# Kernel optimization log

Measured on AMD Instinct MI355X. Metric: run time of the kernel, lower is better.

## Reference

```python
import jax, jax.numpy as jnp
import numpy as np

CHANNELS = 256
NUM_HEADS = 4
NUM_GROUPS = 8
EPS = 1e-5


def setup_inputs() -> dict:
    key = jax.random.key(0)
    ks = jax.random.split(key, 7)
    c = CHANNELS
    x = jax.random.normal(ks[0], (2, c, 16, 16, 16), dtype=jnp.float32)
    # GroupNorm affine params (torch init: weight=1, bias=0)
    norm_w = jnp.ones((c,), dtype=jnp.float32)
    norm_b = jnp.zeros((c,), dtype=jnp.float32)
    # 1x1x1 Conv3d weights stored as [out_ch, in_ch]
    fan = 1.0 / np.sqrt(c)
    qkv_w = jax.random.uniform(ks[1], (3 * c, c), minval=-fan, maxval=fan, dtype=jnp.float32)
    qkv_b = jax.random.uniform(ks[2], (3 * c,), minval=-fan, maxval=fan, dtype=jnp.float32)
    proj_w = jax.random.uniform(ks[3], (c, c), minval=-fan, maxval=fan, dtype=jnp.float32)
    proj_b = jax.random.uniform(ks[4], (c,), minval=-fan, maxval=fan, dtype=jnp.float32)
    return {"x": x, "norm_w": norm_w, "norm_b": norm_b,
            "qkv_w": qkv_w, "qkv_b": qkv_b, "proj_w": proj_w, "proj_b": proj_b}


def _group_norm(x, w, b):
    B, C, D, H, W = x.shape
    g = NUM_GROUPS
    xg = x.reshape(B, g, C // g, D, H, W)
    mean = xg.mean(axis=(2, 3, 4, 5), keepdims=True)
    var = xg.var(axis=(2, 3, 4, 5), keepdims=True)
    xg = (xg - mean) * jax.lax.rsqrt(var + EPS)
    x = xg.reshape(B, C, D, H, W)
    return x * w[None, :, None, None, None] + b[None, :, None, None, None]


def _conv1x1(x, w, b):
    # x: [B, Cin, D, H, W], w: [Cout, Cin]
    y = jnp.einsum('bcdhw,oc->bodhw', x, w)
    return y + b[None, :, None, None, None]


def reference(x, norm_w, norm_b, qkv_w, qkv_b, proj_w, proj_b):
    B, C, D, H, W = x.shape
    N = D * H * W
    hd = C // NUM_HEADS
    x_norm = _group_norm(x, norm_w, norm_b)
    qkv = _conv1x1(x_norm, qkv_w, qkv_b)  # [B, 3C, D, H, W]
    q, k, v = jnp.split(qkv, 3, axis=1)
    q = q.reshape(B, NUM_HEADS, hd, N)
    k = k.reshape(B, NUM_HEADS, hd, N)
    v = v.reshape(B, NUM_HEADS, hd, N)
    scale = hd ** -0.5
    # attn[b,h,n,m] = softmax_m(q[:, :, :, n] . k[:, :, :, m] * scale)
    scores = jnp.einsum('bhcn,bhcm->bhnm', q, k) * scale
    attn = jax.nn.softmax(scores, axis=-1)
    out = jnp.einsum('bhcm,bhnm->bhcn', v, attn)
    out = out.reshape(B, C, D, H, W)
    return _conv1x1(out, proj_w, proj_b) + x
```

## Files before the change

### kernel.cpp

```cpp
#include <hip/hip_runtime.h>
#include <hip/hip_bf16.h>

#define NSP 4096
#define CH 256
#define NB 2
#define NG 8
#define CPG 32
#define NHD 4
#define HDIM 64

typedef unsigned short u16;
typedef unsigned int u32;
typedef __attribute__((ext_vector_type(8))) short bf16x8;
typedef __attribute__((ext_vector_type(2))) float f32x2;
typedef __attribute__((ext_vector_type(4))) float f32x4;
typedef __attribute__((ext_vector_type(16))) float f32x16;
typedef __attribute__((ext_vector_type(2))) unsigned int u32x2;

#define MFMA __builtin_amdgcn_mfma_f32_16x16x32_bf16
#define MFMA32 __builtin_amdgcn_mfma_f32_32x32x16_bf16
#define QSCALE 0.18033688f

__device__ __forceinline__ u16 f2bf(float f) {
    u32 i = __float_as_uint(f);
    u32 r = (i + 0x7FFFu + ((i >> 16) & 1u)) >> 16;
    return (u16)r;
}

__device__ __forceinline__ u32 cvtpk(float a, float b) {
    u32 d;
    asm("v_cvt_pk_bf16_f32 %0, %1, %2" : "=v"(d) : "v"(a), "v"(b));
    return d;
}

__device__ __forceinline__ void dma16(const u16* g, u16* l) {
    __builtin_amdgcn_global_load_lds(
        (const __attribute__((address_space(1))) void*)g,
        (__attribute__((address_space(3))) void*)l, 16, 0, 0);
}

__device__ __forceinline__ void plswap(u32& a, u32& b) {
#if __has_builtin(__builtin_amdgcn_permlane32_swap)
    u32x2 r = __builtin_amdgcn_permlane32_swap(a, b, false, false);
    a = r.x; b = r.y;
#else
    u32 sa = (u32)__shfl_xor((int)a, 32);
    u32 sb = (u32)__shfl_xor((int)b, 32);
    bool hi = (threadIdx.x & 32) != 0;
    u32 na = hi ? sb : a;
    u32 nb = hi ? b : sa;
    a = na; b = nb;
#endif
}

__global__ __launch_bounds__(256) void prep(const float* __restrict__ qw,
                                            const float* __restrict__ pw,
                                            u16* __restrict__ wqb,
                                            u16* __restrict__ wpb,
                                            const float* __restrict__ x,
                                            float* __restrict__ partial) {
    if (blockIdx.x < 256) {
        int i = (blockIdx.x * 256 + threadIdx.x) * 4;
        const float* src; u16* dstbase; int j;
        if (i < 3 * CH * CH) { src = qw + i; dstbase = wqb; j = i; }
        else { j = i - 3 * CH * CH; src = pw + j; dstbase = wpb; }
        int m = j >> 8, c = j & 255;
        int dc = ((((c >> 3) ^ (m & 7)) << 3)) | (c & 7);
        float4 v = *(const float4*)src;
        ushort4 o;
        o.x = f2bf(v.x); o.y = f2bf(v.y); o.z = f2bf(v.z); o.w = f2bf(v.w);
        *(ushort4*)(dstbase + (m << 8) + dc) = o;
        return;
    }
    const int id = blockIdx.x - 256;
    const int bg = id >> 4, chunk = id & 15;
    const float* p = x + (size_t)bg * (CPG * NSP) + chunk * 8192;
    float s = 0.f, ss = 0.f;
    for (int i = threadIdx.x; i < 2048; i += 256) {
        float4 u = ((const float4*)p)[i];
        s += u.x + u.y + u.z + u.w;
        ss += u.x * u.x + u.y * u.y + u.z * u.z + u.w * u.w;
    }
    for (int off = 32; off > 0; off >>= 1) {
        s += __shfl_down(s, off);
        ss += __shfl_down(ss, off);
    }
    __shared__ float red[4][2];
    const int wv = threadIdx.x >> 6;
    if ((threadIdx.x & 63) == 0) { red[wv][0] = s; red[wv][1] = ss; }
    __syncthreads();
    if (threadIdx.x == 0) {
        float ts = red[0][0] + red[1][0] + red[2][0] + red[3][0];
        float tq = red[0][1] + red[1][1] + red[2][1] + red[3][1];
        partial[(bg * 16 + chunk) * 2]     = ts;
        partial[(bg * 16 + chunk) * 2 + 1] = tq;
    }
}

__global__ __launch_bounds__(256) void gn_apply_t(const float* __restrict__ x,
                                                  const float* __restrict__ partial,
                                                  const float* __restrict__ w,
                                                  const float* __restrict__ b,
                                                  u16* __restrict__ xnT) {
    __shared__ u16 T[64][72];
    const int n0 = blockIdx.x * 64, c0 = blockIdx.y * 64, bb = blockIdx.z;
    const int t = threadIdx.x;
    const int rc = t & 63;
    const int g  = t >> 6;
    const int c  = c0 + rc;
    const int bg = bb * NG + c / CPG;
    float s = 0.f, q = 0.f;
#pragma unroll
    for (int j = 0; j < 16; ++j) {
        s += partial[(bg * 16 + j) * 2];
        q += partial[(bg * 16 + j) * 2 + 1];
    }
    const float cnt = (float)(CPG * NSP);
    float mean = s / cnt;
    float var  = q / cnt - mean * mean;
    float rstd = rsqrtf(var + 1e-5f);
    float wf = w[c] * rstd, bv = b[c] - mean * wf;
    const float* px = x + ((size_t)bb * CH + c) * NSP + n0 + g * 16;
#pragma unroll
    for (int i = 0; i < 4; ++i) {
        float4 v = *(const float4*)(px + i * 4);
        T[g * 16 + i * 4 + 0][rc] = f2bf(v.x * wf + bv);
        T[g * 16 + i * 4 + 1][rc] = f2bf(v.y * wf + bv);
        T[g * 16 + i * 4 + 2][rc] = f2bf(v.z * wf + bv);
        T[g * 16 + i * 4 + 3][rc] = f2bf(v.w * wf + bv);
    }
    __syncthreads();
    int n = t >> 2, ch = (t & 3) * 16;
    uint4 o0 = *(const uint4*)&T[n][ch];
    uint4 o1 = *(const uint4*)&T[n][ch + 8];
    const int sw = n & 7;
    const int chunk0 = (c0 + ch) >> 3;
    u16* rowp = xnT + ((size_t)bb * NSP + n0 + n) * CH;
    *(uint4*)(rowp + ((chunk0 ^ sw) << 3))       = o0;
    *(uint4*)(rowp + (((chunk0 + 1) ^ sw) << 3)) = o1;
}

__global__ __launch_bounds__(256, 2) void gemm_qkv(const u16* __restrict__ Aw,
                                                   const float* __restrict__ bias,
                                                   const u16* __restrict__ xnT,
                                                   u16* __restrict__ qT,
                                                   u16* __restrict__ kT,
                                                   u16* __restrict__ v) {
    __shared__ u16 As[64][256];
    __shared__ u16 Bs[64][256];
    const int flat = blockIdx.x + 64 * (blockIdx.y + 12 * blockIdx.z);
    const int xcd = flat & 7, loc = flat >> 3;
    const int mI  = loc % 12;
    const int n16 = xcd * 16 + loc / 12;
    const int n0 = (n16 & 63) * 64, m0 = mI * 64, bb = n16 >> 6;
    const int wave = threadIdx.x >> 6, lane = threadIdx.x & 63;
    const int lq = lane & 15, quad = lane >> 4;
#pragma unroll
    for (int j = 0; j < 8; ++j) {
        int r2 = (wave * 8 + j) * 2;
        dma16(Aw + (size_t)(m0 + r2) * CH + lane * 8, &As[r2][0]);
        dma16(xnT + ((size_t)bb * NSP + n0 + r2) * CH + lane * 8, &Bs[r2][0]);
    }
    __syncthreads();
    const int wm = (wave >> 1) * 32, wn = (wave & 1) * 32;
    const int sw = lq & 7;
    f32x4 acc[2][2] = {};
#pragma unroll
    for (int kk = 0; kk < 8; ++kk) {
        bf16x8 a[2], b[2];
#pragma unroll
        for (int mt = 0; mt < 2; ++mt)
            a[mt] = *(const bf16x8*)&As[wm + mt * 16 + lq][(((kk * 4 + quad) ^ sw)) << 3];
#pragma unroll
        for (int nt = 0; nt < 2; ++nt)
            b[nt] = *(const bf16x8*)&Bs[wn + nt * 16 + lq][(((kk * 4 + quad) ^ sw)) << 3];
#pragma unroll
        for (int mt = 0; mt < 2; ++mt)
#pragma unroll
            for (int nt = 0; nt < 2; ++nt)
                acc[mt][nt] = MFMA(a[mt], b[nt], acc[mt][nt], 0, 0, 0);
    }
    const int sect = m0 >> 8;
    const int h = (m0 & 255) >> 6;
    const float osc = (sect == 0) ? QSCALE : 1.f;
#pragma unroll
    for (int im = 0; im < 2; ++im) {
        int ml = wm + im * 16 + quad * 4;
        float4 bs = *(const float4*)(bias + m0 + ml);
#pragma unroll
        for (int in = 0; in < 2; ++in) {
            int n = n0 + wn + in * 16 + lq;
            f32x4 a = acc[im][in];
            float v0 = (a[0] + bs.x) * osc, v1 = (a[1] + bs.y) * osc;
            float v2 = (a[2] + bs.z) * osc, v3 = (a[3] + bs.w) * osc;
            if (sect < 2) {
                int lc = ml >> 3, sub = ml & 7;
                int colp = ((lc ^ (n & 7)) << 3) | sub;
                u16* base = (sect ? kT : qT) +
                            (((size_t)bb * NHD + h) * NSP + n) * HDIM + colp;
                ushort4 o;
                o.x = f2bf(v0); o.y = f2bf(v1); o.z = f2bf(v2); o.w = f2bf(v3);
                *(ushort4*)base = o;
            } else {
                float vv[4] = {v0, v1, v2, v3};
#pragma unroll
                for (int r = 0; r < 4; ++r) {
                    int ch = (m0 - 512) + ml + r;
                    int pos = (n & ~63) + ((((n >> 3) & 7) ^ (ch & 7)) << 3) + (n & 7);
                    v[((size_t)bb * CH + ch) * NSP + pos] = f2bf(vv[r]);
                }
            }
        }
    }
}

__global__ __launch_bounds__(512, 2) void attn16(const u16* __restrict__ qT,
                                                 const u16* __restrict__ kT,
                                                 const u16* __restrict__ vN,
                                                 u16* __restrict__ aoT) {
    __shared__ __align__(16) char smem[131072];
    u16 (*Ks)[2][64][64] = reinterpret_cast<u16(*)[2][64][64]>(smem);
    u16 (*Vs)[2][64][64] = reinterpret_cast<u16(*)[2][64][64]>(smem + 65536);

    const int id  = blockIdx.x + 32 * (blockIdx.y + 4 * blockIdx.z);
    const int xcd = id & 7, loc = id >> 3;
    const int h = xcd & 3, bb = xcd >> 2;

    const int t = threadIdx.x;
    const int wave = t >> 6, lane = t & 63;
    const int l31 = lane & 31, hi = lane >> 5, ln7 = lane & 7;
    const int qg = wave >> 2;
    const int csl = wave & 3;
    const int q_lo = loc * 128 + qg * 64;

    bf16x8 qf0[4], qf1[4];
    {
        const u16* qrow0 = qT + (((size_t)bb * NHD + h) * NSP + q_lo + l31) * HDIM;
        const u16* qrow1 = qrow0 + 32 * HDIM;
#pragma unroll
        for (int d = 0; d < 4; ++d) {
            qf0[d] = *(const bf16x8*)(qrow0 + (((d * 2 + hi) ^ ln7) << 3));
            qf1[d] = *(const bf16x8*)(qrow1 + (((d * 2 + hi) ^ ln7) << 3));
        }
    }

    const u16* khead = kT + ((size_t)bb * NHD + h) * NSP * (size_t)HDIM;
    const u16* vhead = vN + ((size_t)bb * CH + h * HDIM) * NSP;

    const int sV  = wave >> 2;
    const int ssl = wave & 3;
    int koff[4];
#pragma unroll
    for (int d = 0; d < 4; ++d) koff[d] = (((d * 2 + hi) ^ ln7) << 3);

#pragma unroll
    for (int j = 0; j < 8; ++j) {
        if (sV == 0)
            dma16(khead + (size_t)(ssl * 1024 + j * 8) * HDIM + lane * 8,
                  &Ks[ssl][0][j * 8][0]);
        else
            dma16(vhead + (size_t)(j * 8 + (lane >> 3)) * NSP + ssl * 1024 + (lane & 7) * 8,
                  &Vs[ssl][0][j * 8][0]);
    }

    float l0 = 0.f, l1 = 0.f;
    f32x16 O00 = {}, O01 = {}, O10 = {}, O11 = {};

    auto softmax_pack = [&](const f32x16& s, float& lacc, u32* pfa, u32* pfb) {
        f32x2 a2 = {0.f, 0.f};
        u32 pk0, pk1, pk2, pk3, pk4, pk5, pk6, pk7;
        {
            float p0 = __builtin_amdgcn_exp2f(s[0]),  p1 = __builtin_amdgcn_exp2f(s[1]);
            float p2 = __builtin_amdgcn_exp2f(s[2]),  p3 = __builtin_amdgcn_exp2f(s[3]);
            a2 += (f32x2){p0, p1}; a2 += (f32x2){p2, p3};
            pk0 = cvtpk(p0, p1); pk1 = cvtpk(p2, p3);
        }
        {
            float p0 = __builtin_amdgcn_exp2f(s[4]),  p1 = __builtin_amdgcn_exp2f(s[5]);
            float p2 = __builtin_amdgcn_exp2f(s[6]),  p3 = __builtin_amdgcn_exp2f(s[7]);
            a2 += (f32x2){p0, p1}; a2 += (f32x2){p2, p3};
            pk2 = cvtpk(p0, p1); pk3 = cvtpk(p2, p3);
        }
        {
            float p0 = __builtin_amdgcn_exp2f(s[8]),  p1 = __builtin_amdgcn_exp2f(s[9]);
            float p2 = __builtin_amdgcn_exp2f(s[10]), p3 = __builtin_amdgcn_exp2f(s[11]);
            a2 += (f32x2){p0, p1}; a2 += (f32x2){p2, p3};
            pk4 = cvtpk(p0, p1); pk5 = cvtpk(p2, p3);
        }
        {
            float p0 = __builtin_amdgcn_exp2f(s[12]), p1 = __builtin_amdgcn_exp2f(s[13]);
            float p2 = __builtin_amdgcn_exp2f(s[14]), p3 = __builtin_amdgcn_exp2f(s[15]);
            a2 += (f32x2){p0, p1}; a2 += (f32x2){p2, p3};
            pk6 = cvtpk(p0, p1); pk7 = cvtpk(p2, p3);
        }
        lacc += a2.x + a2.y;
        plswap(pk0, pk2); plswap(pk1, pk3);
        plswap(pk4, pk6); plswap(pk5, pk7);
        pfa[0] = pk0; pfa[1] = pk1; pfa[2] = pk2; pfa[3] = pk3;
        pfb[0] = pk4; pfb[1] = pk5; pfb[2] = pk6; pfb[3] = pk7;
    };

    for (int kt = 0; kt < 16; ++kt) {
        const int cur = kt & 1;
        __syncthreads();
        if (kt < 15) {
            const int K1 = (kt + 1) * 64;
#pragma unroll
            for (int j = 0; j < 8; ++j) {
                if (sV == 0)
                    dma16(khead + (size_t)(ssl * 1024 + K1 + j * 8) * HDIM + lane * 8,
                          &Ks[ssl][cur ^ 1][j * 8][0]);
                else
                    dma16(vhead + (size_t)(j * 8 + (lane >> 3)) * NSP + ssl * 1024 + K1 + (lane & 7) * 8,
                          &Vs[ssl][cur ^ 1][j * 8][0]);
            }
        }
        f32x16 st00 = {}, st01 = {}, st10 = {}, st11 = {};
        {
            bf16x8 kf0 = *(const bf16x8*)&Ks[csl][cur][l31][koff[0]];
            bf16x8 kf1 = *(const bf16x8*)&Ks[csl][cur][l31][koff[1]];
            bf16x8 kf2 = *(const bf16x8*)&Ks[csl][cur][l31][koff[2]];
            bf16x8 kf3 = *(const bf16x8*)&Ks[csl][cur][l31][koff[3]];
            st00 = MFMA32(kf0, qf0[0], st00, 0, 0, 0);
            st00 = MFMA32(kf1, qf0[1], st00, 0, 0, 0);
            st00 = MFMA32(kf2, qf0[2], st00, 0, 0, 0);
            st00 = MFMA32(kf3, qf0[3], st00, 0, 0, 0);
            st01 = MFMA32(kf0, qf1[0], st01, 0, 0, 0);
            st01 = MFMA32(kf1, qf1[1], st01, 0, 0, 0);
            st01 = MFMA32(kf2, qf1[2], st01, 0, 0, 0);
            st01 = MFMA32(kf3, qf1[3], st01, 0, 0, 0);
        }
        {
            bf16x8 kf0 = *(const bf16x8*)&Ks[csl][cur][32 + l31][koff[0]];
            bf16x8 kf1 = *(const bf16x8*)&Ks[csl][cur][32 + l31][koff[1]];
            bf16x8 kf2 = *(const bf16x8*)&Ks[csl][cur][32 + l31][koff[2]];
            bf16x8 kf3 = *(const bf16x8*)&Ks[csl][cur][32 + l31][koff[3]];
            st10 = MFMA32(kf0, qf0[0], st10, 0, 0, 0);
            st10 = MFMA32(kf1, qf0[1], st10, 0, 0, 0);
            st10 = MFMA32(kf2, qf0[2], st10, 0, 0, 0);
            st10 = MFMA32(kf3, qf0[3], st10, 0, 0, 0);
            st11 = MFMA32(kf0, qf1[0], st11, 0, 0, 0);
            st11 = MFMA32(kf1, qf1[1], st11, 0, 0, 0);
            st11 = MFMA32(kf2, qf1[2], st11, 0, 0, 0);
            st11 = MFMA32(kf3, qf1[3], st11, 0, 0, 0);
        }
#pragma unroll
        for (int ktile = 0; ktile < 2; ++ktile) {
            bf16x8 vf00 = *(const bf16x8*)&Vs[csl][cur][l31][(((ktile * 4 + hi) ^ ln7) << 3)];
            bf16x8 vf01 = *(const bf16x8*)&Vs[csl][cur][l31][(((ktile * 4 + 2 + hi) ^ ln7) << 3)];
            bf16x8 vf10 = *(const bf16x8*)&Vs[csl][cur][32 + l31][(((ktile * 4 + hi) ^ ln7) << 3)];
            bf16x8 vf11 = *(const bf16x8*)&Vs[csl][cur][32 + l31][(((ktile * 4 + 2 + hi) ^ ln7) << 3)];
            u32 pA0[4], pB0[4], pA1[4], pB1[4];
            softmax_pack(ktile ? st10 : st00, l0, pA0, pB0);
            softmax_pack(ktile ? st11 : st01, l1, pA1, pB1);
            bf16x8 a0 = *(const bf16x8*)pA0, b0 = *(const bf16x8*)pB0;
            bf16x8 a1 = *(const bf16x8*)pA1, b1 = *(const bf16x8*)pB1;
            O00 = MFMA32(vf00, a0, O00, 0, 0, 0);
            O00 = MFMA32(vf01, b0, O00, 0, 0, 0);
            O10 = MFMA32(vf00, a1, O10, 0, 0, 0);
            O10 = MFMA32(vf01, b1, O10, 0, 0, 0);
            O01 = MFMA32(vf10, a0, O01, 0, 0, 0);
            O01 = MFMA32(vf11, b0, O01, 0, 0, 0);
            O11 = MFMA32(vf10, a1, O11, 0, 0, 0);
            O11 = MFMA32(vf11, b1, O11, 0, 0, 0);
        }
    }
    l0 += __shfl_xor(l0, 32);
    l1 += __shfl_xor(l1, 32);
    __syncthreads();
    float* ob  = (float*)smem;
    float* MlA = (float*)(smem + 65536);
    if (lane < 32) {
        MlA[(wave * 2 + 0) * 32 + l31] = l0;
        MlA[(wave * 2 + 1) * 32 + l31] = l1;
    }
    auto stash = [&](float* sp, int f, const f32x16& o) {
#pragma unroll
        for (int cc = 0; cc < 4; ++cc) {
            f32x4 tmp = {o[4 * cc + 0], o[4 * cc + 1], o[4 * cc + 2], o[4 * cc + 3]};
            *(f32x4*)(sp + ((f * 4 + cc) * 64 + lane) * 4) = tmp;
        }
    };
    auto absorb = [&](const float* sp, int f, f32x16& o) {
#pragma unroll
        for (int cc = 0; cc < 4; ++cc) {
            f32x4 tmp = *(const f32x4*)(sp + ((f * 4 + cc) * 64 + lane) * 4);
            o[4 * cc + 0] += tmp[0]; o[4 * cc + 1] += tmp[1];
            o[4 * cc + 2] += tmp[2]; o[4 * cc + 3] += tmp[3];
        }
    };
    if (csl >= 2) {
        float* sp = ob + (qg * 2 + (csl - 2)) * 4096;
        stash(sp, 0, O00); stash(sp, 1, O01); stash(sp, 2, O10); stash(sp, 3, O11);
    }
    __syncthreads();
    if (csl < 2) {
        float* sp = ob + (qg * 2 + csl) * 4096;
        absorb(sp, 0, O00); absorb(sp, 1, O01); absorb(sp, 2, O10); absorb(sp, 3, O11);
    }
    __syncthreads();
    if (csl == 1) {
        float* sp = ob + qg * 4096;
        stash(sp, 0, O00); stash(sp, 1, O01); stash(sp, 2, O10); stash(sp, 3, O11);
    }
    __syncthreads();
    if (csl == 0) {
        float* sp = ob + qg * 4096;
        absorb(sp, 0, O00); absorb(sp, 1, O01); absorb(sp, 2, O10); absorb(sp, 3, O11);
        float gl0 = l0 + MlA[((qg * 4 + 1) * 2 + 0) * 32 + l31]
                       + MlA[((qg * 4 + 2) * 2 + 0) * 32 + l31]
                       + MlA[((qg * 4 + 3) * 2 + 0) * 32 + l31];
        float gl1 = l1 + MlA[((qg * 4 + 1) * 2 + 1) * 32 + l31]
                       + MlA[((qg * 4 + 2) * 2 + 1) * 32 + l31]
                       + MlA[((qg * 4 + 3) * 2 + 1) * 32 + l31];
        float linv0 = 1.f / gl0, linv1 = 1.f / gl1;
        auto emit = [&](const f32x16& oc0, const f32x16& oc1, float linv, int qtrow) {
            u16* rowp = aoT + ((size_t)bb * NSP + q_lo + qtrow * 32 + l31) * CH;
#pragma unroll
            for (int ct = 0; ct < 2; ++ct) {
                const f32x16& oc = ct ? oc1 : oc0;
#pragma unroll
                for (int g = 0; g < 4; ++g) {
                    ushort4 o;
                    o.x = f2bf(oc[4 * g + 0] * linv);
                    o.y = f2bf(oc[4 * g + 1] * linv);
                    o.z = f2bf(oc[4 * g + 2] * linv);
                    o.w = f2bf(oc[4 * g + 3] * linv);
                    int chunk = h * 8 + ct * 4 + g;
                    *(ushort4*)(rowp + ((chunk ^ ln7) << 3) + (hi << 2)) = o;
                }
            }
        };
        emit(O00, O01, linv0, 0);
        emit(O10, O11, linv1, 1);
    }
}

__global__ __launch_bounds__(256, 2) void gemm_proj(const u16* __restrict__ Aw,
                                                    const float* __restrict__ bias,
                                                    const u16* __restrict__ aoT,
                                                    const float* __restrict__ xres,
                                                    float* __restrict__ out) {
    __shared__ u16 As[64][256];
    __shared__ u16 Bs[64][256];
    const int flat = blockIdx.x + 64 * (blockIdx.y + 4 * blockIdx.z);
    const int xcd = flat & 7, loc = flat >> 3;
    const int mI  = loc & 3;
    const int n16 = xcd * 16 + (loc >> 2);
    const int n0 = (n16 & 63) * 64, m0 = mI * 64, bb = n16 >> 6;
    const int wave = threadIdx.x >> 6, lane = threadIdx.x & 63;
    const int lq = lane & 15, quad = lane >> 4;
#pragma unroll
    for (int j = 0; j < 8; ++j) {
        int r2 = (wave * 8 + j) * 2;
        dma16(Aw + (size_t)(m0 + r2) * CH + lane * 8, &As[r2][0]);
        dma16(aoT + ((size_t)bb * NSP + n0 + r2) * CH + lane * 8, &Bs[r2][0]);
    }
    __syncthreads();
    const int wm = (wave >> 1) * 32, wn = (wave & 1) * 32;
    const int sw = lq & 7;
    f32x4 acc[2][2] = {};
#pragma unroll
    for (int kk = 0; kk < 8; ++kk) {
        bf16x8 a[2], b[2];
#pragma unroll
        for (int mt = 0; mt < 2; ++mt)
            a[mt] = *(const bf16x8*)&As[wm + mt * 16 + lq][(((kk * 4 + quad) ^ sw)) << 3];
#pragma unroll
        for (int nt = 0; nt < 2; ++nt)
            b[nt] = *(const bf16x8*)&Bs[wn + nt * 16 + lq][(((kk * 4 + quad) ^ sw)) << 3];
#pragma unroll
        for (int mt = 0; mt < 2; ++mt)
#pragma unroll
            for (int nt = 0; nt < 2; ++nt)
                acc[mt][nt] = MFMA(a[mt], b[nt], acc[mt][nt], 0, 0, 0);
    }
#pragma unroll
    for (int im = 0; im < 2; ++im) {
        int ml = wm + im * 16 + quad * 4;
        float4 bs = *(const float4*)(bias + m0 + ml);
        float bsv[4] = {bs.x, bs.y, bs.z, bs.w};
#pragma unroll
        for (int in = 0; in < 2; ++in) {
            int n = n0 + wn + in * 16 + lq;
            f32x4 a = acc[im][in];
#pragma unroll
            for (int r = 0; r < 4; ++r) {
                size_t idx = ((size_t)bb * CH + m0 + ml + r) * NSP + n;
                out[idx] = a[r] + bsv[r] + xres[idx];
            }
        }
    }
}

extern "C" void kernel_launch(void* const* d_in, const int* in_sizes, int n_in,
                              void* d_out, int out_size, void* d_ws, size_t ws_size,
                              hipStream_t stream) {
    const float* x      = (const float*)d_in[0];
    const float* norm_w = (const float*)d_in[1];
    const float* norm_b = (const float*)d_in[2];
    const float* qkv_w  = (const float*)d_in[3];
    const float* qkv_b  = (const float*)d_in[4];
    const float* proj_w = (const float*)d_in[5];
    const float* proj_b = (const float*)d_in[6];
    float* out = (float*)d_out;

    char* w = (char*)d_ws;
    float* partial = (float*)w;
    u16* wqb = (u16*)(w + 4096);
    u16* wpb = (u16*)(w + 4096 + 393216);
    u16* xnT = (u16*)(w + 528384);
    u16* qT  = (u16*)(w + 528384 + 4194304);
    u16* kT  = (u16*)(w + 528384 + 2 * 4194304);
    u16* v   = (u16*)(w + 528384 + 3 * 4194304);
    u16* aoT = xnT;

    prep<<<dim3(512), 256, 0, stream>>>(qkv_w, proj_w, wqb, wpb, x, partial);
    gn_apply_t<<<dim3(NSP / 64, CH / 64, NB), 256, 0, stream>>>(
        x, partial, norm_w, norm_b, xnT);
    gemm_qkv<<<dim3(NSP / 64, (3 * CH) / 64, NB), 256, 0, stream>>>(
        wqb, qkv_b, xnT, qT, kT, v);
    attn16<<<dim3(NSP / 128, NHD, NB), 512, 0, stream>>>(qT, kT, v, aoT);
    gemm_proj<<<dim3(NSP / 64, CH / 64, NB), 256, 0, stream>>>(
        wpb, proj_b, aoT, x, out);
}
```

Before: 135.7 us.

## Split each attention wave's key tile across two waves in 1024-thread blocks

The attention kernel now launches 1024 threads per block instead of 512. Each pair of waves splits the 64-key tile into two 32-key halves, and the DMA load work is split between them. This halves per-wave score and softmax work and lowers register pressure, which is meant to improve latency hiding through more waves in flight. In exchange the cross-wave output reduction grows to three stash/absorb rounds with more barriers, and occupancy is bounded at one block per CU.

```diff
diff --git a/kernel.cpp b/kernel.cpp
--- a/kernel.cpp
+++ b/kernel.cpp
@@ -214,10 +214,10 @@
     }
 }
 
-__global__ __launch_bounds__(512, 2) void attn16(const u16* __restrict__ qT,
-                                                 const u16* __restrict__ kT,
-                                                 const u16* __restrict__ vN,
-                                                 u16* __restrict__ aoT) {
+__global__ __launch_bounds__(1024, 1) void attn17(const u16* __restrict__ qT,
+                                                  const u16* __restrict__ kT,
+                                                  const u16* __restrict__ vN,
+                                                  u16* __restrict__ aoT) {
     __shared__ __align__(16) char smem[131072];
     u16 (*Ks)[2][64][64] = reinterpret_cast<u16(*)[2][64][64]>(smem);
     u16 (*Vs)[2][64][64] = reinterpret_cast<u16(*)[2][64][64]>(smem + 65536);
@@ -229,8 +229,10 @@
     const int t = threadIdx.x;
     const int wave = t >> 6, lane = t & 63;
     const int l31 = lane & 31, hi = lane >> 5, ln7 = lane & 7;
-    const int qg = wave >> 2;
-    const int csl = wave & 3;
+    const int qg  = wave >> 3;
+    const int csl = (wave >> 1) & 3;
+    const int kth = wave & 1;
+    const int mi  = (csl << 1) | kth;
     const int q_lo = loc * 128 + qg * 64;
 
     bf16x8 qf0[4], qf1[4];
@@ -247,20 +249,22 @@
     const u16* khead = kT + ((size_t)bb * NHD + h) * NSP * (size_t)HDIM;
     const u16* vhead = vN + ((size_t)bb * CH + h * HDIM) * NSP;
 
-    const int sV  = wave >> 2;
-    const int ssl = wave & 3;
+    const int sV    = wave >> 3;
+    const int ssl   = (wave >> 1) & 3;
+    const int rbase = (wave & 1) * 32;
     int koff[4];
 #pragma unroll
     for (int d = 0; d < 4; ++d) koff[d] = (((d * 2 + hi) ^ ln7) << 3);
 
 #pragma unroll
-    for (int j = 0; j < 8; ++j) {
+    for (int j = 0; j < 4; ++j) {
+        int r8 = rbase + j * 8;
         if (sV == 0)
-            dma16(khead + (size_t)(ssl * 1024 + j * 8) * HDIM + lane * 8,
-                  &Ks[ssl][0][j * 8][0]);
+            dma16(khead + (size_t)(ssl * 1024 + r8) * HDIM + lane * 8,
+                  &Ks[ssl][0][r8][0]);
         else
-            dma16(vhead + (size_t)(j * 8 + (lane >> 3)) * NSP + ssl * 1024 + (lane & 7) * 8,
-                  &Vs[ssl][0][j * 8][0]);
+            dma16(vhead + (size_t)(r8 + (lane >> 3)) * NSP + ssl * 1024 + (lane & 7) * 8,
+                  &Vs[ssl][0][r8][0]);
     }
 
     float l0 = 0.f, l1 = 0.f;
@@ -306,74 +310,67 @@
         if (kt < 15) {
             const int K1 = (kt + 1) * 64;
 #pragma unroll
-            for (int j = 0; j < 8; ++j) {
+            for (int j = 0; j < 4; ++j) {
+                int r8 = rbase + j * 8;
                 if (sV == 0)
-                    dma16(khead + (size_t)(ssl * 1024 + K1 + j * 8) * HDIM + lane * 8,
-                          &Ks[ssl][cur ^ 1][j * 8][0]);
+                    dma16(khead + (size_t)(ssl * 1024 + K1 + r8) * HDIM + lane * 8,
+                          &Ks[ssl][cur ^ 1][r8][0]);
                 else
-                    dma16(vhead + (size_t)(j * 8 + (lane >> 3)) * NSP + ssl * 1024 + K1 + (lane & 7) * 8,
-                          &Vs[ssl][cur ^ 1][j * 8][0]);
+                    dma16(vhead + (size_t)(r8 + (lane >> 3)) * NSP + ssl * 1024 + K1 + (lane & 7) * 8,
+                          &Vs[ssl][cur ^ 1][r8][0]);
             }
         }
-        f32x16 st00 = {}, st01 = {}, st10 = {}, st11 = {};
+        f32x16 st0 = {}, st1 = {};
         {
-            bf16x8 kf0 = *(const bf16x8*)&Ks[csl][cur][l31][koff[0]];
-            bf16x8 kf1 = *(const bf16x8*)&Ks[csl][cur][l31][koff[1]];
-            bf16x8 kf2 = *(const bf16x8*)&Ks[csl][cur][l31][koff[2]];
-            bf16x8 kf3 = *(const bf16x8*)&Ks[csl][cur][l31][koff[3]];
-            st00 = MFMA32(kf0, qf0[0], st00, 0, 0, 0);
-            st00 = MFMA32(kf1, qf0[1], st00, 0, 0, 0);
-            st00 = MFMA32(kf2, qf0[2], st00, 0, 0, 0);
-            st00 = MFMA32(kf3, qf0[3], st00, 0, 0, 0);
-            st01 = MFMA32(kf0, qf1[0], st01, 0, 0, 0);
-            st01 = MFMA32(kf1, qf1[1], st01, 0, 0, 0);
-            st01 = MFMA32(kf2, qf1[2], st01, 0, 0, 0);
-            st01 = MFMA32(kf3, qf1[3], st01, 0, 0, 0);
-        }
-        {
-            bf16x8 kf0 = *(const bf16x8*)&Ks[csl][cur][32 + l31][koff[0]];
-            bf16x8 kf1 = *(const bf16x8*)&Ks[csl][cur][32 + l31][koff[1]];
-            bf16x8 kf2 = *(const bf16x8*)&Ks[csl][cur][32 + l31][koff[2]];
-            bf16x8 kf3 = *(const bf16x8*)&Ks[csl][cur][32 + l31][koff[3]];
-            st10 = MFMA32(kf0, qf0[0], st10, 0, 0, 0);
-            st10 = MFMA32(kf1, qf0[1], st10, 0, 0, 0);
-            st10 = MFMA32(kf2, qf0[2], st10, 0, 0, 0);
-            st10 = MFMA32(kf3, qf0[3], st10, 0, 0, 0);
-            st11 = MFMA32(kf0, qf1[0], st11, 0, 0, 0);
-            st11 = MFMA32(kf1, qf1[1], st11, 0, 0, 0);
-            st11 = MFMA32(kf2, qf1[2], st11, 0, 0, 0);
-            st11 = MFMA32(kf3, qf1[3], st11, 0, 0, 0);
-        }
-#pragma unroll
-        for (int ktile = 0; ktile < 2; ++ktile) {
-            bf16x8 vf00 = *(const bf16x8*)&Vs[csl][cur][l31][(((ktile * 4 + hi) ^ ln7) << 3)];
-            bf16x8 vf01 = *(const bf16x8*)&Vs[csl][cur][l31][(((ktile * 4 + 2 + hi) ^ ln7) << 3)];
-            bf16x8 vf10 = *(const bf16x8*)&Vs[csl][cur][32 + l31][(((ktile * 4 + hi) ^ ln7) << 3)];
-            bf16x8 vf11 = *(const bf16x8*)&Vs[csl][cur][32 + l31][(((ktile * 4 + 2 + hi) ^ ln7) << 3)];
-            u32 pA0[4], pB0[4], pA1[4], pB1[4];
-            softmax_pack(ktile ? st10 : st00, l0, pA0, pB0);
-            softmax_pack(ktile ? st11 : st01, l1, pA1, pB1);
-            bf16x8 a0 = *(const bf16x8*)pA0, b0 = *(const bf16x8*)pB0;
-            bf16x8 a1 = *(const bf16x8*)pA1, b1 = *(const bf16x8*)pB1;
-            O00 = MFMA32(vf00, a0, O00, 0, 0, 0);
-            O00 = MFMA32(vf01, b0, O00, 0, 0, 0);
-            O10 = MFMA32(vf00, a1, O10, 0, 0, 0);
-            O10 = MFMA32(vf01, b1, O10, 0, 0, 0);
-            O01 = MFMA32(vf10, a0, O01, 0, 0, 0);
-            O01 = MFMA32(vf11, b0, O01, 0, 0, 0);
-            O11 = MFMA32(vf10, a1, O11, 0, 0, 0);
-            O11 = MFMA32(vf11, b1, O11, 0, 0, 0);
-        }
+            bf16x8 kf0 = *(const bf16x8*)&Ks[csl][cur][kth * 32 + l31][koff[0]];
+            bf16x8 kf1 = *(const bf16x8*)&Ks[csl][cur][kth * 32 + l31][koff[1]];
+            bf16x8 kf2 = *(const bf16x8*)&Ks[csl][cur][kth * 32 + l31][koff[2]];
+            bf16x8 kf3 = *(const bf16x8*)&Ks[csl][cur][kth * 32 + l31][koff[3]];
+            st0 = MFMA32(kf0, qf0[0], st0, 0, 0, 0);
+            st0 = MFMA32(kf1, qf0[1], st0, 0, 0, 0);
+            st0 = MFMA32(kf2, qf0[2], st0, 0, 0, 0);
+            st0 = MFMA32(kf3, qf0[3], st0, 0, 0, 0);
+            st1 = MFMA32(kf0, qf1[0], st1, 0, 0, 0);
+            st1 = MFMA32(kf1, qf1[1], st1, 0, 0, 0);
+            st1 = MFMA32(kf2, qf1[2], st1, 0, 0, 0);
+            st1 = MFMA32(kf3, qf1[3], st1, 0, 0, 0);
+        }
+        bf16x8 vf00 = *(const bf16x8*)&Vs[csl][cur][l31][(((kth * 4 + hi) ^ ln7) << 3)];
+        bf16x8 vf01 = *(const bf16x8*)&Vs[csl][cur][l31][(((kth * 4 + 2 + hi) ^ ln7) << 3)];
+        bf16x8 vf10 = *(const bf16x8*)&Vs[csl][cur][32 + l31][(((kth * 4 + hi) ^ ln7) << 3)];
+        bf16x8 vf11 = *(const bf16x8*)&Vs[csl][cur][32 + l31][(((kth * 4 + 2 + hi) ^ ln7) << 3)];
+        u32 pA0[4], pB0[4], pA1[4], pB1[4];
+        softmax_pack(st0, l0, pA0, pB0);
+        softmax_pack(st1, l1, pA1, pB1);
+        bf16x8 a0 = *(const bf16x8*)pA0, b0 = *(const bf16x8*)pB0;
+        bf16x8 a1 = *(const bf16x8*)pA1, b1 = *(const bf16x8*)pB1;
+        O00 = MFMA32(vf00, a0, O00, 0, 0, 0);
+        O00 = MFMA32(vf01, b0, O00, 0, 0, 0);
+        O10 = MFMA32(vf00, a1, O10, 0, 0, 0);
+        O10 = MFMA32(vf01, b1, O10, 0, 0, 0);
+        O01 = MFMA32(vf10, a0, O01, 0, 0, 0);
+        O01 = MFMA32(vf11, b0, O01, 0, 0, 0);
+        O11 = MFMA32(vf10, a1, O11, 0, 0, 0);
+        O11 = MFMA32(vf11, b1, O11, 0, 0, 0);
     }
     l0 += __shfl_xor(l0, 32);
     l1 += __shfl_xor(l1, 32);
-    __syncthreads();
-    float* ob  = (float*)smem;
-    float* MlA = (float*)(smem + 65536);
+    float* MlA = (float*)smem;
     if (lane < 32) {
-        MlA[(wave * 2 + 0) * 32 + l31] = l0;
-        MlA[(wave * 2 + 1) * 32 + l31] = l1;
-    }
+        MlA[((qg * 8 + mi) * 2 + 0) * 32 + l31] = l0;
+        MlA[((qg * 8 + mi) * 2 + 1) * 32 + l31] = l1;
+    }
+    __syncthreads();
+    float gl0 = 0.f, gl1 = 0.f;
+    if (mi == 0) {
+#pragma unroll
+        for (int m = 0; m < 8; ++m) {
+            gl0 += MlA[((qg * 8 + m) * 2 + 0) * 32 + l31];
+            gl1 += MlA[((qg * 8 + m) * 2 + 1) * 32 + l31];
+        }
+    }
+    __syncthreads();
+    float* ob = (float*)smem;
     auto stash = [&](float* sp, int f, const f32x16& o) {
 #pragma unroll
         for (int cc = 0; cc < 4; ++cc) {
@@ -389,30 +386,24 @@
             o[4 * cc + 2] += tmp[2]; o[4 * cc + 3] += tmp[3];
         }
     };
-    if (csl >= 2) {
-        float* sp = ob + (qg * 2 + (csl - 2)) * 4096;
+    auto stash4 = [&](float* sp) {
         stash(sp, 0, O00); stash(sp, 1, O01); stash(sp, 2, O10); stash(sp, 3, O11);
-    }
-    __syncthreads();
-    if (csl < 2) {
-        float* sp = ob + (qg * 2 + csl) * 4096;
+    };
+    auto absorb4 = [&](const float* sp) {
         absorb(sp, 0, O00); absorb(sp, 1, O01); absorb(sp, 2, O10); absorb(sp, 3, O11);
-    }
-    __syncthreads();
-    if (csl == 1) {
-        float* sp = ob + qg * 4096;
-        stash(sp, 0, O00); stash(sp, 1, O01); stash(sp, 2, O10); stash(sp, 3, O11);
-    }
-    __syncthreads();
-    if (csl == 0) {
-        float* sp = ob + qg * 4096;
-        absorb(sp, 0, O00); absorb(sp, 1, O01); absorb(sp, 2, O10); absorb(sp, 3, O11);
-        float gl0 = l0 + MlA[((qg * 4 + 1) * 2 + 0) * 32 + l31]
-                       + MlA[((qg * 4 + 2) * 2 + 0) * 32 + l31]
-                       + MlA[((qg * 4 + 3) * 2 + 0) * 32 + l31];
-        float gl1 = l1 + MlA[((qg * 4 + 1) * 2 + 1) * 32 + l31]
-                       + MlA[((qg * 4 + 2) * 2 + 1) * 32 + l31]
-                       + MlA[((qg * 4 + 3) * 2 + 1) * 32 + l31];
+    };
+    if (mi & 1) stash4(ob + (qg * 4 + (mi >> 1)) * 4096);
+    __syncthreads();
+    if (!(mi & 1)) absorb4(ob + (qg * 4 + (mi >> 1)) * 4096);
+    __syncthreads();
+    if (mi == 2 || mi == 6) stash4(ob + (qg * 2 + (mi >> 2)) * 4096);
+    __syncthreads();
+    if (mi == 0 || mi == 4) absorb4(ob + (qg * 2 + (mi >> 2)) * 4096);
+    __syncthreads();
+    if (mi == 4) stash4(ob + qg * 4096);
+    __syncthreads();
+    if (mi == 0) {
+        absorb4(ob + qg * 4096);
         float linv0 = 1.f / gl0, linv1 = 1.f / gl1;
         auto emit = [&](const f32x16& oc0, const f32x16& oc1, float linv, int qtrow) {
             u16* rowp = aoT + ((size_t)bb * NSP + q_lo + qtrow * 32 + l31) * CH;
@@ -520,7 +511,7 @@
         x, partial, norm_w, norm_b, xnT);
     gemm_qkv<<<dim3(NSP / 64, (3 * CH) / 64, NB), 256, 0, stream>>>(
         wqb, qkv_b, xnT, qT, kT, v);
-    attn16<<<dim3(NSP / 128, NHD, NB), 512, 0, stream>>>(qT, kT, v, aoT);
+    attn17<<<dim3(NSP / 128, NHD, NB), 1024, 0, stream>>>(qT, kT, v, aoT);
     gemm_proj<<<dim3(NSP / 64, CH / 64, NB), 256, 0, stream>>>(
         wpb, proj_b, aoT, x, out);
 }
```

After: 219.9 us. +62.0%, slower.

## Load K and V fragments directly from global memory instead of LDS staging

Applied to the files above, without the earlier changes.

The attention kernel stops staging K and V tiles through double-buffered shared memory with async DMA and per-iteration barriers. Each wave now reads its K rows and V columns straight from global memory (relying on L2/cache) into MFMA fragments, and LDS shrinks to what the final reduction needs. This removes the __syncthreads per key tile and the LDS round trip, and may allow more occupancy. In exchange it loses explicit prefetch overlap and depends on the cache serving repeated K/V reads across waves and blocks.

```diff
diff --git a/kernel.cpp b/kernel.cpp
--- a/kernel.cpp
+++ b/kernel.cpp
@@ -214,13 +214,11 @@
     }
 }
 
-__global__ __launch_bounds__(512, 2) void attn16(const u16* __restrict__ qT,
+__global__ __launch_bounds__(512, 2) void attn18(const u16* __restrict__ qT,
                                                  const u16* __restrict__ kT,
                                                  const u16* __restrict__ vN,
                                                  u16* __restrict__ aoT) {
-    __shared__ __align__(16) char smem[131072];
-    u16 (*Ks)[2][64][64] = reinterpret_cast<u16(*)[2][64][64]>(smem);
-    u16 (*Vs)[2][64][64] = reinterpret_cast<u16(*)[2][64][64]>(smem + 65536);
+    __shared__ __align__(16) char smem[67584];
 
     const int id  = blockIdx.x + 32 * (blockIdx.y + 4 * blockIdx.z);
     const int xcd = id & 7, loc = id >> 3;
@@ -247,21 +245,14 @@
     const u16* khead = kT + ((size_t)bb * NHD + h) * NSP * (size_t)HDIM;
     const u16* vhead = vN + ((size_t)bb * CH + h * HDIM) * NSP;
 
-    const int sV  = wave >> 2;
-    const int ssl = wave & 3;
     int koff[4];
 #pragma unroll
     for (int d = 0; d < 4; ++d) koff[d] = (((d * 2 + hi) ^ ln7) << 3);
 
-#pragma unroll
-    for (int j = 0; j < 8; ++j) {
-        if (sV == 0)
-            dma16(khead + (size_t)(ssl * 1024 + j * 8) * HDIM + lane * 8,
-                  &Ks[ssl][0][j * 8][0]);
-        else
-            dma16(vhead + (size_t)(j * 8 + (lane >> 3)) * NSP + ssl * 1024 + (lane & 7) * 8,
-                  &Vs[ssl][0][j * 8][0]);
-    }
+    const u16* krow0 = khead + (size_t)(csl * 1024 + l31) * HDIM;
+    const u16* krow1 = khead + (size_t)(csl * 1024 + 32 + l31) * HDIM;
+    const u16* vrow0 = vhead + (size_t)l31 * NSP + csl * 1024;
+    const u16* vrow1 = vhead + (size_t)(32 + l31) * NSP + csl * 1024;
 
     float l0 = 0.f, l1 = 0.f;
     f32x16 O00 = {}, O01 = {}, O10 = {}, O11 = {};
@@ -301,26 +292,14 @@
     };
 
     for (int kt = 0; kt < 16; ++kt) {
-        const int cur = kt & 1;
-        __syncthreads();
-        if (kt < 15) {
-            const int K1 = (kt + 1) * 64;
-#pragma unroll
-            for (int j = 0; j < 8; ++j) {
-                if (sV == 0)
-                    dma16(khead + (size_t)(ssl * 1024 + K1 + j * 8) * HDIM + lane * 8,
-                          &Ks[ssl][cur ^ 1][j * 8][0]);
-                else
-                    dma16(vhead + (size_t)(j * 8 + (lane >> 3)) * NSP + ssl * 1024 + K1 + (lane & 7) * 8,
-                          &Vs[ssl][cur ^ 1][j * 8][0]);
-            }
-        }
+        const int kb = kt * 64;
         f32x16 st00 = {}, st01 = {}, st10 = {}, st11 = {};
         {
-            bf16x8 kf0 = *(const bf16x8*)&Ks[csl][cur][l31][koff[0]];
-            bf16x8 kf1 = *(const bf16x8*)&Ks[csl][cur][l31][koff[1]];
-            bf16x8 kf2 = *(const bf16x8*)&Ks[csl][cur][l31][koff[2]];
-            bf16x8 kf3 = *(const bf16x8*)&Ks[csl][cur][l31][koff[3]];
+            const u16* kr = krow0 + (size_t)kb * HDIM;
+            bf16x8 kf0 = *(const bf16x8*)(kr + koff[0]);
+            bf16x8 kf1 = *(const bf16x8*)(kr + koff[1]);
+            bf16x8 kf2 = *(const bf16x8*)(kr + koff[2]);
+            bf16x8 kf3 = *(const bf16x8*)(kr + koff[3]);
             st00 = MFMA32(kf0, qf0[0], st00, 0, 0, 0);
             st00 = MFMA32(kf1, qf0[1], st00, 0, 0, 0);
             st00 = MFMA32(kf2, qf0[2], st00, 0, 0, 0);
@@ -331,10 +310,11 @@
             st01 = MFMA32(kf3, qf1[3], st01, 0, 0, 0);
         }
         {
-            bf16x8 kf0 = *(const bf16x8*)&Ks[csl][cur][32 + l31][koff[0]];
-            bf16x8 kf1 = *(const bf16x8*)&Ks[csl][cur][32 + l31][koff[1]];
-            bf16x8 kf2 = *(const bf16x8*)&Ks[csl][cur][32 + l31][koff[2]];
-            bf16x8 kf3 = *(const bf16x8*)&Ks[csl][cur][32 + l31][koff[3]];
+            const u16* kr = krow1 + (size_t)kb * HDIM;
+            bf16x8 kf0 = *(const bf16x8*)(kr + koff[0]);
+            bf16x8 kf1 = *(const bf16x8*)(kr + koff[1]);
+            bf16x8 kf2 = *(const bf16x8*)(kr + koff[2]);
+            bf16x8 kf3 = *(const bf16x8*)(kr + koff[3]);
             st10 = MFMA32(kf0, qf0[0], st10, 0, 0, 0);
             st10 = MFMA32(kf1, qf0[1], st10, 0, 0, 0);
             st10 = MFMA32(kf2, qf0[2], st10, 0, 0, 0);
@@ -346,10 +326,10 @@
         }
 #pragma unroll
         for (int ktile = 0; ktile < 2; ++ktile) {
-            bf16x8 vf00 = *(const bf16x8*)&Vs[csl][cur][l31][(((ktile * 4 + hi) ^ ln7) << 3)];
-            bf16x8 vf01 = *(const bf16x8*)&Vs[csl][cur][l31][(((ktile * 4 + 2 + hi) ^ ln7) << 3)];
-            bf16x8 vf10 = *(const bf16x8*)&Vs[csl][cur][32 + l31][(((ktile * 4 + hi) ^ ln7) << 3)];
-            bf16x8 vf11 = *(const bf16x8*)&Vs[csl][cur][32 + l31][(((ktile * 4 + 2 + hi) ^ ln7) << 3)];
+            bf16x8 vf00 = *(const bf16x8*)(vrow0 + kb + (((ktile * 4 + hi) ^ ln7) << 3));
+            bf16x8 vf01 = *(const bf16x8*)(vrow0 + kb + (((ktile * 4 + 2 + hi) ^ ln7) << 3));
+            bf16x8 vf10 = *(const bf16x8*)(vrow1 + kb + (((ktile * 4 + hi) ^ ln7) << 3));
+            bf16x8 vf11 = *(const bf16x8*)(vrow1 + kb + (((ktile * 4 + 2 + hi) ^ ln7) << 3));
             u32 pA0[4], pB0[4], pA1[4], pB1[4];
             softmax_pack(ktile ? st10 : st00, l0, pA0, pB0);
             softmax_pack(ktile ? st11 : st01, l1, pA1, pB1);
@@ -367,7 +347,6 @@
     }
     l0 += __shfl_xor(l0, 32);
     l1 += __shfl_xor(l1, 32);
-    __syncthreads();
     float* ob  = (float*)smem;
     float* MlA = (float*)(smem + 65536);
     if (lane < 32) {
@@ -520,7 +499,7 @@
         x, partial, norm_w, norm_b, xnT);
     gemm_qkv<<<dim3(NSP / 64, (3 * CH) / 64, NB), 256, 0, stream>>>(
         wqb, qkv_b, xnT, qT, kT, v);
-    attn16<<<dim3(NSP / 128, NHD, NB), 512, 0, stream>>>(qT, kT, v, aoT);
+    attn18<<<dim3(NSP / 128, NHD, NB), 512, 0, stream>>>(qT, kT, v, aoT);
     gemm_proj<<<dim3(NSP / 64, CH / 64, NB), 256, 0, stream>>>(
         wpb, proj_b, aoT, x, out);
 }
```

After: 139.2 us. +2.6%, slower.
